# Performance work log

Hardware: AMD Instinct MI355X
Metric: run time of the kernel (lower is better)

The kernel has to match this reference:

```python
import jax, jax.numpy as jnp
import numpy as np

N, D = 8192, 128


def setup_inputs() -> dict:
    key = jax.random.key(0)
    k1, k2 = jax.random.split(key)
    emb = jax.random.normal(k1, (N, D), dtype=jnp.float32)
    graphWeight = jax.random.uniform(k2, (N, N), dtype=jnp.float32)
    return {"emb": emb, "graphWeight": graphWeight}


def _pairwise_l2(x):
    # cdist(x, x, p=2) via the ||a-b||^2 = ||a||^2 + ||b||^2 - 2 a.b identity.
    sq_norms = jnp.sum(x * x, axis=-1)  # [N]
    sq = sq_norms[:, None] + sq_norms[None, :] - 2.0 * (x @ x.T)  # [N, N]
    sq = jnp.maximum(sq, 0.0)
    # safe sqrt (grad-safe at exactly-zero distances, e.g. the diagonal)
    return jnp.where(sq > 0.0, jnp.sqrt(jnp.where(sq > 0.0, sq, 1.0)), 0.0)


def reference(emb, graphWeight):
    dist = _pairwise_l2(emb)                 # [N, N]
    dist = dist / jnp.max(dist)              # normalize by global max
    return jnp.mean((1.0 - dist) * graphWeight)  # scalar loss
```

## Files before the change

### kernel.cpp

```cpp
#include <hip/hip_runtime.h>
#include <hip/hip_bf16.h>

#define NN 8192
#define DD 128
#define JTPB 16
#define NBLK 512

typedef __attribute__((ext_vector_type(8))) short short8;
typedef __attribute__((ext_vector_type(4))) float f32x4;

__device__ __forceinline__ unsigned short f2bf(float x) {
    unsigned u = __float_as_uint(x);
    u += 0x7FFFu + ((u >> 16) & 1u);
    return (unsigned short)(u >> 16);
}
__device__ __forceinline__ float bf2f(unsigned short b) {
    return __uint_as_float(((unsigned)b) << 16);
}

__device__ __forceinline__ void gld_lds16(const float* src, float* ldst) {
    __builtin_amdgcn_global_load_lds(
        (const __attribute__((address_space(1))) void*)src,
        (__attribute__((address_space(3))) void*)ldst, 16, 0, 0);
}

__global__ void prep_kernel(const float* __restrict__ emb,
                            unsigned short* __restrict__ ebf,
                            float* __restrict__ nrm,
                            unsigned int* __restrict__ done) {
    if (blockIdx.x == 0 && threadIdx.x == 0)
        __hip_atomic_store(done, 0u, __ATOMIC_RELAXED, __HIP_MEMORY_SCOPE_AGENT);
    int row  = blockIdx.x * 4 + (threadIdx.x >> 6);
    int lane = threadIdx.x & 63;
    const float2 v = *reinterpret_cast<const float2*>(emb + (size_t)row * DD + lane * 2);
    unsigned short b0 = f2bf(v.x), b1 = f2bf(v.y);
    ushort2 st; st.x = b0; st.y = b1;
    *reinterpret_cast<ushort2*>(ebf + (size_t)row * DD + lane * 2) = st;
    float f0 = bf2f(b0), f1 = bf2f(b1);
    float s = f0 * f0 + f1 * f1;
    #pragma unroll
    for (int m = 32; m; m >>= 1) s += __shfl_xor(s, m);
    if (lane == 0) nrm[row] = s;
}

__global__ __launch_bounds__(256, 2)
void gram_kernel(const unsigned short* __restrict__ ebf,
                 const float* __restrict__ nrm,
                 const float* __restrict__ W,
                 float4* __restrict__ part,
                 unsigned int* __restrict__ done,
                 float* __restrict__ out) {
    __shared__ float wlds[2][64 * 128];
    __shared__ float sw_s[4], sdw_s[4], dm_s[4];
    __shared__ double swd[4], sdwd[4];
    __shared__ float dmf[4];
    __shared__ int last_s;

    const int wave = threadIdx.x >> 6;
    const int lane = threadIdx.x & 63;
    const int wRow = wave >> 1;
    const int wCol = wave & 1;
    const int i0  = blockIdx.y * 128;
    const int jc0 = blockIdx.x * (JTPB * 64);

    const int lr = lane & 15;
    const int hi = lane >> 4;
    const int lk = hi * 8;

    int pj[8], pc[8];
    #pragma unroll
    for (int r = 0; r < 8; ++r) {
        int q = r * 256 + (int)threadIdx.x;
        int jrow = q >> 5;
        pj[r] = jrow;
        pc[r] = ((q & 31) ^ (jrow & 7)) * 4;
    }

    short8 af[4][4];
    #pragma unroll
    for (int kc = 0; kc < 4; ++kc)
        #pragma unroll
        for (int m = 0; m < 4; ++m)
            af[kc][m] = *reinterpret_cast<const short8*>(
                ebf + (size_t)(i0 + wRow * 64 + m * 16 + lr) * DD + kc * 32 + lk);
    f32x4 ni4[4];
    #pragma unroll
    for (int m = 0; m < 4; ++m)
        ni4[m] = *reinterpret_cast<const f32x4*>(nrm + i0 + wRow * 64 + m * 16 + hi * 4);

    __builtin_amdgcn_sched_barrier(0);
    #pragma unroll
    for (int r = 0; r < 8; ++r)
        gld_lds16(W + (size_t)(jc0 + pj[r]) * NN + i0 + pc[r],
                  &wlds[0][r * 1024 + wave * 256]);
    __syncthreads();

    float sW = 0.f, sDW = 0.f, dmax = 0.f;

    for (int t = 0; t < JTPB; ++t) {
        const int j0t = jc0 + t * 64;
        const int jw  = j0t + wCol * 32;
        const int cb  = t & 1;

        short8 bf[4][2];
        #pragma unroll
        for (int kc = 0; kc < 4; ++kc)
            #pragma unroll
            for (int n = 0; n < 2; ++n)
                bf[kc][n] = *reinterpret_cast<const short8*>(
                    ebf + (size_t)(jw + n * 16 + lr) * DD + kc * 32 + lk);
        float nj[2];
        #pragma unroll
        for (int n = 0; n < 2; ++n) nj[n] = nrm[jw + n * 16 + lr];

        __builtin_amdgcn_sched_barrier(0);
        if (t + 1 < JTPB) {
            #pragma unroll
            for (int r = 0; r < 8; ++r)
                gld_lds16(W + (size_t)(j0t + 64 + pj[r]) * NN + i0 + pc[r],
                          &wlds[cb ^ 1][r * 1024 + wave * 256]);
        }
        __builtin_amdgcn_sched_barrier(0);

        f32x4 acc[4][2];
        #pragma unroll
        for (int m = 0; m < 4; ++m)
            #pragma unroll
            for (int n = 0; n < 2; ++n) acc[m][n] = (f32x4){0.f, 0.f, 0.f, 0.f};
        #pragma unroll
        for (int kc = 0; kc < 4; ++kc)
            #pragma unroll
            for (int m = 0; m < 4; ++m)
                #pragma unroll
                for (int n = 0; n < 2; ++n)
                    acc[m][n] = __builtin_amdgcn_mfma_f32_16x16x32_bf16(
                        af[kc][m], bf[kc][n], acc[m][n], 0, 0, 0);

        #pragma unroll
        for (int m = 0; m < 4; ++m) {
            #pragma unroll
            for (int n = 0; n < 2; ++n) {
                const int jp = wCol * 32 + n * 16 + lr;
                const int c0 = wRow * 16 + m * 4 + hi;
                const f32x4 w4 = *reinterpret_cast<const f32x4*>(
                    &wlds[cb][jp * 128 + ((c0 ^ (jp & 7)) * 4)]);
                #pragma unroll
                for (int r = 0; r < 4; ++r) {
                    float sq = ni4[m][r] + nj[n] - 2.0f * acc[m][n][r];
                    sq = fmaxf(sq, 0.0f);
                    float d = sqrtf(sq);
                    sW  += w4[r];
                    sDW += w4[r] * d;
                    dmax = fmaxf(dmax, d);
                }
            }
        }
        __syncthreads();
    }

    #pragma unroll
    for (int m = 32; m; m >>= 1) {
        sW  += __shfl_xor(sW, m);
        sDW += __shfl_xor(sDW, m);
        dmax = fmaxf(dmax, __shfl_xor(dmax, m));
    }
    if (lane == 0) { sw_s[wave] = sW; sdw_s[wave] = sDW; dm_s[wave] = dmax; }
    __syncthreads();

    const int bid = blockIdx.y * gridDim.x + blockIdx.x;
    if (threadIdx.x == 0) {
        float SW = 0.f, SDW = 0.f, DM = 0.f;
        #pragma unroll
        for (int k = 0; k < 4; ++k) {
            SW += sw_s[k]; SDW += sdw_s[k]; DM = fmaxf(DM, dm_s[k]);
        }
        float4 p; p.x = SW; p.y = SDW; p.z = DM; p.w = 0.f;
        part[bid] = p;
        __threadfence();
        unsigned prev = atomicAdd(done, 1u);
        last_s = (prev == NBLK - 1) ? 1 : 0;
    }
    __syncthreads();

    if (last_s) {
        __threadfence();
        double SW = 0.0, SDW = 0.0;
        float DM = 0.f;
        for (int idx = threadIdx.x; idx < NBLK; idx += 256) {
            const float* p = reinterpret_cast<const float*>(part + idx);
            float x = __hip_atomic_load(p + 0, __ATOMIC_RELAXED, __HIP_MEMORY_SCOPE_AGENT);
            float y = __hip_atomic_load(p + 1, __ATOMIC_RELAXED, __HIP_MEMORY_SCOPE_AGENT);
            float z = __hip_atomic_load(p + 2, __ATOMIC_RELAXED, __HIP_MEMORY_SCOPE_AGENT);
            SW += (double)x; SDW += (double)y; DM = fmaxf(DM, z);
        }
        #pragma unroll
        for (int m = 32; m; m >>= 1) {
            SW  += __shfl_xor(SW, m);
            SDW += __shfl_xor(SDW, m);
            DM = fmaxf(DM, __shfl_xor(DM, m));
        }
        if (lane == 0) { swd[wave] = SW; sdwd[wave] = SDW; dmf[wave] = DM; }
        __syncthreads();
        if (threadIdx.x == 0) {
            double TSW = 0.0, TSDW = 0.0; float TDM = 0.f;
            #pragma unroll
            for (int k = 0; k < 4; ++k) {
                TSW += swd[k]; TSDW += sdwd[k]; TDM = fmaxf(TDM, dmf[k]);
            }
            out[0] = (float)((TSW - TSDW / (double)TDM) / ((double)NN * (double)NN));
        }
    }
}

extern "C" void kernel_launch(void* const* d_in, const int* in_sizes, int n_in,
                              void* d_out, int out_size, void* d_ws, size_t ws_size,
                              hipStream_t stream) {
    const float* emb = (const float*)d_in[0];
    const float* W   = (const float*)d_in[1];
    float* out = (float*)d_out;

    char* ws = (char*)d_ws;
    float4* part        = (float4*)ws;
    unsigned int* done  = (unsigned int*)(ws + 8192);
    unsigned short* ebf = (unsigned short*)(ws + 16384);
    float* nrm          = (float*)(ws + 16384 + (size_t)NN * DD * 2);

    prep_kernel<<<NN / 4, 256, 0, stream>>>(emb, ebf, nrm, done);
    dim3 grid(NN / (64 * JTPB), NN / 128);
    gram_kernel<<<grid, 256, 0, stream>>>(ebf, nrm, W, part, done, out);
}
```

Baseline: 83.99 us.

## Reshape block tile to 256 i-rows by 32 j-cols with shared B fragments

Changes the per-block tile from 128 i by 64 j per step to 256 i by 32 j per step. Each wave now owns a distinct 64-row i slice, and all four waves share the same 32 j-columns. The W staging is rewritten to match, with 32 rows of 256 floats per buffer, 1 KiB contiguous per row, and a new XOR swizzle. The aim is to make W loads longer and more contiguous and to cut redundant B-fragment loads per block, at the cost of more j steps per column chunk, since the grid keeps the same block count.

```diff
diff --git a/kernel.cpp b/kernel.cpp
--- a/kernel.cpp
+++ b/kernel.cpp
@@ -50,7 +50,7 @@
                  float4* __restrict__ part,
                  unsigned int* __restrict__ done,
                  float* __restrict__ out) {
-    __shared__ float wlds[2][64 * 128];
+    __shared__ float wlds[2][32 * 256];
     __shared__ float sw_s[4], sdw_s[4], dm_s[4];
     __shared__ double swd[4], sdwd[4];
     __shared__ float dmf[4];
@@ -58,23 +58,23 @@
 
     const int wave = threadIdx.x >> 6;
     const int lane = threadIdx.x & 63;
-    const int wRow = wave >> 1;
-    const int wCol = wave & 1;
-    const int i0  = blockIdx.y * 128;
-    const int jc0 = blockIdx.x * (JTPB * 64);
-
     const int lr = lane & 15;
     const int hi = lane >> 4;
     const int lk = hi * 8;
 
-    int pj[8], pc[8];
-    #pragma unroll
-    for (int r = 0; r < 8; ++r) {
-        int q = r * 256 + (int)threadIdx.x;
-        int jrow = q >> 5;
-        pj[r] = jrow;
-        pc[r] = ((q & 31) ^ (jrow & 7)) * 4;
-    }
+    const int i0  = blockIdx.y * 256;
+    const int jc0 = blockIdx.x * (JTPB * 32);
+
+    auto stage = [&](int j0t, int buf) {
+        float* dst = &wlds[buf][0];
+        #pragma unroll
+        for (int r = 0; r < 8; ++r) {
+            const int row = r * 4 + wave;
+            const int csw = lane ^ (row & 7);
+            gld_lds16(W + (size_t)(j0t + row) * NN + i0 + csw * 4,
+                      dst + r * 1024 + wave * 256);
+        }
+    };
 
     short8 af[4][4];
     #pragma unroll
@@ -82,24 +82,20 @@
         #pragma unroll
         for (int m = 0; m < 4; ++m)
             af[kc][m] = *reinterpret_cast<const short8*>(
-                ebf + (size_t)(i0 + wRow * 64 + m * 16 + lr) * DD + kc * 32 + lk);
+                ebf + (size_t)(i0 + wave * 64 + m * 16 + lr) * DD + kc * 32 + lk);
     f32x4 ni4[4];
     #pragma unroll
     for (int m = 0; m < 4; ++m)
-        ni4[m] = *reinterpret_cast<const f32x4*>(nrm + i0 + wRow * 64 + m * 16 + hi * 4);
+        ni4[m] = *reinterpret_cast<const f32x4*>(nrm + i0 + wave * 64 + m * 16 + hi * 4);
 
     __builtin_amdgcn_sched_barrier(0);
-    #pragma unroll
-    for (int r = 0; r < 8; ++r)
-        gld_lds16(W + (size_t)(jc0 + pj[r]) * NN + i0 + pc[r],
-                  &wlds[0][r * 1024 + wave * 256]);
+    stage(jc0, 0);
     __syncthreads();
 
     float sW = 0.f, sDW = 0.f, dmax = 0.f;
 
     for (int t = 0; t < JTPB; ++t) {
-        const int j0t = jc0 + t * 64;
-        const int jw  = j0t + wCol * 32;
+        const int j0t = jc0 + t * 32;
         const int cb  = t & 1;
 
         short8 bf[4][2];
@@ -108,18 +104,13 @@
             #pragma unroll
             for (int n = 0; n < 2; ++n)
                 bf[kc][n] = *reinterpret_cast<const short8*>(
-                    ebf + (size_t)(jw + n * 16 + lr) * DD + kc * 32 + lk);
+                    ebf + (size_t)(j0t + n * 16 + lr) * DD + kc * 32 + lk);
         float nj[2];
         #pragma unroll
-        for (int n = 0; n < 2; ++n) nj[n] = nrm[jw + n * 16 + lr];
+        for (int n = 0; n < 2; ++n) nj[n] = nrm[j0t + n * 16 + lr];
 
         __builtin_amdgcn_sched_barrier(0);
-        if (t + 1 < JTPB) {
-            #pragma unroll
-            for (int r = 0; r < 8; ++r)
-                gld_lds16(W + (size_t)(j0t + 64 + pj[r]) * NN + i0 + pc[r],
-                          &wlds[cb ^ 1][r * 1024 + wave * 256]);
-        }
+        if (t + 1 < JTPB) stage(j0t + 32, cb ^ 1);
         __builtin_amdgcn_sched_barrier(0);
 
         f32x4 acc[4][2];
@@ -140,10 +131,10 @@
         for (int m = 0; m < 4; ++m) {
             #pragma unroll
             for (int n = 0; n < 2; ++n) {
-                const int jp = wCol * 32 + n * 16 + lr;
-                const int c0 = wRow * 16 + m * 4 + hi;
+                const int jp = n * 16 + lr;
+                const int c0 = wave * 16 + m * 4 + hi;
                 const f32x4 w4 = *reinterpret_cast<const f32x4*>(
-                    &wlds[cb][jp * 128 + ((c0 ^ (jp & 7)) * 4)]);
+                    &wlds[cb][jp * 256 + ((c0 ^ (jp & 7)) * 4)]);
                 #pragma unroll
                 for (int r = 0; r < 4; ++r) {
                     float sq = ni4[m][r] + nj[n] - 2.0f * acc[m][n][r];
@@ -226,6 +217,6 @@
     float* nrm          = (float*)(ws + 16384 + (size_t)NN * DD * 2);
 
     prep_kernel<<<NN / 4, 256, 0, stream>>>(emb, ebf, nrm, done);
-    dim3 grid(NN / (64 * JTPB), NN / 128);
+    dim3 grid(NN / (32 * JTPB), NN / 256);
     gram_kernel<<<grid, 256, 0, stream>>>(ebf, nrm, W, part, done, out);
 }
```

Result: no change. 83.79 us (-0.2%).
